# Kernel tuning notes

Hardware: AMD Instinct MI355X
Metric: run time of the kernel (lower is better)

The kernel has to match this reference:

```python
import jax, jax.numpy as jnp
import numpy as np
from jax import lax

K = 3
STRIDE = 1
PAD = 1


def _active_sites(mask):
    # mask: [B, Cm, H, W] int. A patch is 'active' if ANY element of the
    # unfolded (im2col) patch is nonzero -> max-pool of (mask != 0) over the
    # same kernel/stride/padding window.
    m = jnp.any(mask != 0, axis=1, keepdims=True).astype(jnp.float32)  # [B,1,H,W]
    pooled = lax.reduce_window(
        m, 0.0, lax.max,
        window_dimensions=(1, 1, K, K),
        window_strides=(1, 1, STRIDE, STRIDE),
        padding=((0, 0), (0, 0), (PAD, PAD), (PAD, PAD)))
    return pooled > 0  # [B,1,H_out,W_out] bool


def reference(x, mask, weight, bias):
    # Faithful math of MyConv: conv2d(x, weight) + bias at active patch sites
    # (patches whose mask window contains any nonzero), exact zeros elsewhere.
    # masked_scatter in the original preserves patch order, so this equals
    # active * (conv + bias).
    conv = lax.conv_general_dilated(
        x, weight,
        window_strides=(STRIDE, STRIDE),
        padding=((PAD, PAD), (PAD, PAD)),
        dimension_numbers=('NCHW', 'OIHW', 'NCHW'))  # [B,C_out,H_out,W_out]
    active = _active_sites(mask)
    out = (conv + bias[None, :, None, None]) * active.astype(conv.dtype)
    return out


def setup_inputs() -> dict:
    key = jax.random.key(0)
    k1, k2, k3, k4 = jax.random.split(key, 4)
    B, C_in, C_out, H, W = 8, 128, 128, 128, 128
    x = jax.random.normal(k1, (B, C_in, H, W), dtype=jnp.float32)
    mask = jax.random.randint(k2, (B, 1, H, W), 0, 2, dtype=jnp.int32)
    fan_in = C_in * K * K
    bound = 1.0 / np.sqrt(fan_in)
    weight = jax.random.uniform(k3, (C_out, C_in, K, K), minval=-bound, maxval=bound, dtype=jnp.float32)
    bias = jax.random.uniform(k4, (C_out,), minval=-bound, maxval=bound, dtype=jnp.float32)
    return {"x": x, "mask": mask, "weight": weight, "bias": bias}
```

## Files before the change

kernel.cpp:

```cpp
#include <hip/hip_runtime.h>


typedef __bf16 bf16x8 __attribute__((ext_vector_type(8)));
typedef unsigned short u16x8 __attribute__((ext_vector_type(8)));
typedef float f32x4 __attribute__((ext_vector_type(4)));

__device__ __forceinline__ unsigned short f2bf(float f) {
    unsigned int u = __float_as_uint(f);
    u += 0x7fffu + ((u >> 16) & 1u);
    return (unsigned short)(u >> 16);
}

__global__ void setup_all(const float* __restrict__ x, const float* __restrict__ wgt,
                          unsigned short* __restrict__ xp, unsigned short* __restrict__ wpp) {
    __shared__ float Lf[32 * 132];
    const int t   = threadIdx.x;
    const int bid = blockIdx.x;

    if (bid >= 4160) {
        const int e    = (bid - 4160) * 256 + t;
        const int j    = e & 31;
        const int m    = (e >> 5) & 127;
        const int r    = e >> 12;
        const int kw   = r - (r / 3) * 3;
        const int cbkh = r / 3;
        const int cb   = cbkh & 3;
        const int kh   = cbkh >> 2;
        wpp[e] = f2bf(wgt[((m * 128 + cb * 32 + j) * 3 + kh) * 3 + kw]);
        return;
    }

    const int hh2 = bid % 130;
    const int cb  = (bid / 130) & 3;
    const int b   = bid / 520;
    u16x8* slab = (u16x8*)(xp + (size_t)(((b * 4 + cb) * 130 + hh2)) * 4160);
    const u16x8 z = {0, 0, 0, 0, 0, 0, 0, 0};

    if (hh2 == 0 || hh2 == 129) {
        for (int k = t; k < 520; k += 256) slab[k] = z;
        return;
    }
    const int h = hh2 - 1;

    #pragma unroll
    for (int u = 0; u < 4; ++u) {
        const int f  = t + 256 * u;
        const int ci = f >> 5;
        const int w4 = f & 31;
        const float4 v = *(const float4*)(x + (((b * 128 + cb * 32 + ci) * 128 + h) << 7) + (w4 << 2));
        *(float4*)&Lf[ci * 132 + (w4 << 2)] = v;
    }
    __syncthreads();

    for (int k = t; k < 520; k += 256) {
        const int r = k >> 2;
        const int c = k & 3;
        u16x8 o;
        if (r == 0 || r == 129) {
            o = z;
        } else {
            const int w   = r - 1;
            const int ci0 = (c ^ ((r + (r >> 2)) & 3)) << 3;
            #pragma unroll
            for (int s = 0; s < 8; ++s) o[s] = f2bf(Lf[(ci0 + s) * 132 + w]);
        }
        slab[k] = o;
    }
}

__device__ __forceinline__ void stage_slab(const unsigned char* gx, unsigned char* ls, int t) {
    const int g    = t >> 6;
    const int lane = t & 63;
    #pragma unroll
    for (int u = 0; u < 2; ++u)
        __builtin_amdgcn_global_load_lds(
            (const __attribute__((address_space(1))) unsigned int*)(gx + u * 4096 + g * 1024 + lane * 16),
            (__attribute__((address_space(3))) unsigned int*)(ls + u * 4096 + g * 1024),
            16, 0, 0);
    if (t < 8)
        __builtin_amdgcn_global_load_lds(
            (const __attribute__((address_space(1))) unsigned int*)(gx + 8192 + t * 16),
            (__attribute__((address_space(3))) unsigned int*)(ls + 8192),
            16, 0, 0);
}

__global__ __launch_bounds__(256, 4)
void myconv6(const unsigned short* __restrict__ xp,
             const int* __restrict__ mask,
             const unsigned short* __restrict__ wp,
             const float* __restrict__ bias,
             float* __restrict__ out)
{
    __shared__ __align__(16) unsigned char Xs[2][8320];
    __shared__ float act[128];

    const int t = threadIdx.x;
    const int b = blockIdx.x >> 7;
    const int h = blockIdx.x & 127;

    const int lane = t & 63;
    const int l16  = lane & 15;
    const int q    = lane >> 4;
    const int g    = t >> 6;
    const int mh   = g & 1;
    const int nh   = g >> 1;

    const unsigned char* xpB = (const unsigned char*)xp;

    stage_slab(xpB + (size_t)((b * 4 + 0) * 130 + h + 0) * 8320, &Xs[0][0], t);

    if (t < 128) {
        int any = 0;
        #pragma unroll
        for (int kh = 0; kh < 3; ++kh) {
            int hh = h + kh - 1;
            if ((unsigned)hh < 128u) {
                const int* mrow = mask + (b * 128 + hh) * 128;
                #pragma unroll
                for (int kw = 0; kw < 3; ++kw) {
                    int ww = t + kw - 1;
                    if ((unsigned)ww < 128u) any |= mrow[ww];
                }
            }
        }
        act[t] = any ? 1.0f : 0.0f;
    }

    int bb[3];
    #pragma unroll
    for (int kw = 0; kw < 3; ++kw) {
        const int rr   = l16 + kw;
        const int slot = q ^ ((rr + (rr >> 2)) & 3);
        bb[kw] = nh * 4096 + rr * 64 + (slot << 4);
    }

    const unsigned char* agl = (const unsigned char*)wp + (mh * 64 + l16) * 64 + q * 16;

    f32x4 acc[4][4];
    const f32x4 fzero = {0.f, 0.f, 0.f, 0.f};
    #pragma unroll
    for (int i = 0; i < 4; ++i)
        #pragma unroll
        for (int j = 0; j < 4; ++j)
            acc[i][j] = fzero;

    __syncthreads();

    for (int r = 0; r < 12; ++r) {
        if (r < 11) {
            const int rn = r + 1;
            stage_slab(xpB + (size_t)((b * 4 + (rn & 3)) * 130 + h + (rn >> 2)) * 8320,
                       &Xs[(rn & 1)][0], t);
        }

        const unsigned char* ar = agl + r * 24576;
        const unsigned char* xb = &Xs[r & 1][0];
        #pragma unroll
        for (int kw = 0; kw < 3; ++kw) {
            bf16x8 af[4];
            #pragma unroll
            for (int i = 0; i < 4; ++i)
                af[i] = *(const bf16x8*)(ar + kw * 8192 + i * 1024);
            bf16x8 bfr[4];
            #pragma unroll
            for (int j = 0; j < 4; ++j)
                bfr[j] = *(const bf16x8*)(xb + bb[kw] + j * 1024);
            #pragma unroll
            for (int i = 0; i < 4; ++i)
                #pragma unroll
                for (int j = 0; j < 4; ++j)
                    acc[i][j] = __builtin_amdgcn_mfma_f32_16x16x32_bf16(af[i], bfr[j], acc[i][j], 0, 0, 0);
        }

        __syncthreads();
    }

    #pragma unroll
    for (int i = 0; i < 4; ++i) {
        const int m0 = mh * 64 + (i << 4) + (q << 2);
        const f32x4 bv = *(const f32x4*)(bias + m0);
        #pragma unroll
        for (int j = 0; j < 4; ++j) {
            const int w = nh * 64 + (j << 4) + l16;
            const float a = act[w];
            float* base = out + (((b << 7) + m0) << 14) + (h << 7) + w;
            #pragma unroll
            for (int rg = 0; rg < 4; ++rg)
                base[rg << 14] = (acc[i][j][rg] + bv[rg]) * a;
        }
    }
}

#define LDAF 40
__global__ __launch_bounds__(256, 2)
void myconv_fb(const float* __restrict__ x,
               const int* __restrict__ mask,
               const float* __restrict__ wgt,
               const float* __restrict__ bias,
               float* __restrict__ out)
{
    __shared__ unsigned short As[128 * LDAF];
    __shared__ unsigned short Bs[128 * LDAF];
    __shared__ float act[128];

    const int t   = threadIdx.x;
    const int blk = blockIdx.x;
    const int b   = blk >> 7;
    const int h   = blk & 127;

    if (t < 128) {
        int any = 0;
        #pragma unroll
        for (int kh = 0; kh < 3; ++kh) {
            int hh = h + kh - 1;
            if ((unsigned)hh < 128u) {
                const int* mrow = mask + (b * 128 + hh) * 128;
                #pragma unroll
                for (int kw = 0; kw < 3; ++kw) {
                    int ww = t + kw - 1;
                    if ((unsigned)ww < 128u) any |= mrow[ww];
                }
            }
        }
        act[t] = any ? 1.0f : 0.0f;
    }

    const int lane = t & 63;
    const int l16  = lane & 15;
    const int half = lane >> 4;
    const int wv   = t >> 6;
    const int wm   = (wv >> 1) << 6;
    const int wn   = (wv & 1) << 6;

    f32x4 acc[4][4];
    const f32x4 fzero = {0.f, 0.f, 0.f, 0.f};
    #pragma unroll
    for (int i = 0; i < 4; ++i)
        #pragma unroll
        for (int j = 0; j < 4; ++j)
            acc[i][j] = fzero;

    const int am  = t >> 3;
    const int ac4 = (t & 7) << 2;
    const int n     = t & 127;
    const int khalf = __builtin_amdgcn_readfirstlane(t >> 7);
    const int xb    = b << 21;

    for (int kt = 0; kt < 36; ++kt) {
        __syncthreads();
        #pragma unroll
        for (int jj = 0; jj < 4; ++jj) {
            const int m = am + (jj << 5);
            const float4 v = *(const float4*)(wgt + m * 1152 + kt * 32 + ac4);
            unsigned short* dst = &As[m * LDAF + ac4];
            dst[0] = f2bf(v.x); dst[1] = f2bf(v.y); dst[2] = f2bf(v.z); dst[3] = f2bf(v.w);
        }
        u16x8 bv0, bv1;
        #pragma unroll
        for (int s = 0; s < 16; ++s) {
            const int k  = kt * 32 + khalf * 16 + s;
            const int ci = (k * 7282) >> 16;
            const int r  = k - ci * 9;
            const int kh = (r >= 3) + (r >= 6);
            const int kw = r - kh * 3;
            const int hh = h + kh - 1;
            float v = 0.f;
            if ((unsigned)hh < 128u) {
                const int ww = n + kw - 1;
                if ((unsigned)ww < 128u)
                    v = x[xb + (ci << 14) + (hh << 7) + ww];
            }
            if (s < 8) bv0[s] = f2bf(v); else bv1[s - 8] = f2bf(v);
        }
        *(u16x8*)&Bs[n * LDAF + khalf * 16]     = bv0;
        *(u16x8*)&Bs[n * LDAF + khalf * 16 + 8] = bv1;

        __syncthreads();

        bf16x8 af[4], bfr[4];
        #pragma unroll
        for (int i = 0; i < 4; ++i)
            af[i] = *(const bf16x8*)&As[(wm + (i << 4) + l16) * LDAF + (half << 3)];
        #pragma unroll
        for (int j = 0; j < 4; ++j)
            bfr[j] = *(const bf16x8*)&Bs[(wn + (j << 4) + l16) * LDAF + (half << 3)];
        #pragma unroll
        for (int i = 0; i < 4; ++i)
            #pragma unroll
            for (int j = 0; j < 4; ++j)
                acc[i][j] = __builtin_amdgcn_mfma_f32_16x16x32_bf16(af[i], bfr[j], acc[i][j], 0, 0, 0);
    }

    #pragma unroll
    for (int i = 0; i < 4; ++i) {
        #pragma unroll
        for (int j = 0; j < 4; ++j) {
            const int ncol = wn + (j << 4) + l16;
            const float a  = act[ncol];
            #pragma unroll
            for (int rg = 0; rg < 4; ++rg) {
                const int m = wm + (i << 4) + (half << 2) + rg;
                out[(((b << 7) + m) << 14) + (h << 7) + ncol] =
                    (acc[i][j][rg] + bias[m]) * a;
            }
        }
    }
}

extern "C" void kernel_launch(void* const* d_in, const int* in_sizes, int n_in,
                              void* d_out, int out_size, void* d_ws, size_t ws_size,
                              hipStream_t stream) {
    const float* x    = (const float*)d_in[0];
    const int*   mask = (const int*)d_in[1];
    const float* wgt  = (const float*)d_in[2];
    const float* bias = (const float*)d_in[3];
    float* out        = (float*)d_out;

    const size_t XP_ELEMS = 4160ull * 4160;
    const size_t WP_ELEMS = 36ull * 128 * 32;
    const size_t need = (XP_ELEMS + WP_ELEMS) * 2;

    if (ws_size >= need) {
        unsigned short* xpw = (unsigned short*)d_ws;
        unsigned short* wpw = xpw + XP_ELEMS;
        setup_all<<<dim3(4736), dim3(256), 0, stream>>>(x, wgt, xpw, wpw);
        myconv6<<<dim3(1024), dim3(256), 0, stream>>>(xpw, mask, wpw, bias, out);
    } else {
        myconv_fb<<<dim3(1024), dim3(256), 0, stream>>>(x, mask, wgt, bias, out);
    }
}
```

Measured before the change: 158.8 us.

## Triple-buffer input slabs with prefetch distance two and hoisted weight loads

The conv kernel moves from double to triple buffering of the LDS input slab and prefetches two reduction steps ahead. All three kw weight fragments are loaded at the top of each step, and the loop's __syncthreads is replaced by explicit vmcnt/lgkmcnt waits plus raw barriers. The goal is to hide global-to-LDS latency behind the MFMA work. In exchange it uses more LDS and registers, lowers launch bounds occupancy from 4 to 3, and depends on a hand-counted vmcnt(18) being correct.

```diff
diff --git a/kernel.cpp b/kernel.cpp
--- a/kernel.cpp
+++ b/kernel.cpp
@@ -68,30 +68,29 @@
     }
 }
 
-__device__ __forceinline__ void stage_slab(const unsigned char* gx, unsigned char* ls, int t) {
+__device__ __forceinline__ void stage_slab3(const unsigned char* gx, unsigned char* ls, int t) {
     const int g    = t >> 6;
     const int lane = t & 63;
-    #pragma unroll
-    for (int u = 0; u < 2; ++u)
+    __builtin_amdgcn_global_load_lds(
+        (const __attribute__((address_space(1))) unsigned int*)(gx + g * 1024 + lane * 16),
+        (__attribute__((address_space(3))) unsigned int*)(ls + g * 1024), 16, 0, 0);
+    __builtin_amdgcn_global_load_lds(
+        (const __attribute__((address_space(1))) unsigned int*)(gx + 4096 + g * 1024 + lane * 16),
+        (__attribute__((address_space(3))) unsigned int*)(ls + 4096 + g * 1024), 16, 0, 0);
+    if (lane < 2)
         __builtin_amdgcn_global_load_lds(
-            (const __attribute__((address_space(1))) unsigned int*)(gx + u * 4096 + g * 1024 + lane * 16),
-            (__attribute__((address_space(3))) unsigned int*)(ls + u * 4096 + g * 1024),
-            16, 0, 0);
-    if (t < 8)
-        __builtin_amdgcn_global_load_lds(
-            (const __attribute__((address_space(1))) unsigned int*)(gx + 8192 + t * 16),
-            (__attribute__((address_space(3))) unsigned int*)(ls + 8192),
-            16, 0, 0);
-}
-
-__global__ __launch_bounds__(256, 4)
-void myconv6(const unsigned short* __restrict__ xp,
+            (const __attribute__((address_space(1))) unsigned int*)(gx + 8192 + g * 32 + lane * 16),
+            (__attribute__((address_space(3))) unsigned int*)(ls + 8192 + g * 32), 16, 0, 0);
+}
+
+__global__ __launch_bounds__(256, 3)
+void myconv7(const unsigned short* __restrict__ xp,
              const int* __restrict__ mask,
              const unsigned short* __restrict__ wp,
              const float* __restrict__ bias,
              float* __restrict__ out)
 {
-    __shared__ __align__(16) unsigned char Xs[2][8320];
+    __shared__ __align__(16) unsigned char Xs[3][8320];
     __shared__ float act[128];
 
     const int t = threadIdx.x;
@@ -106,8 +105,6 @@
     const int nh   = g >> 1;
 
     const unsigned char* xpB = (const unsigned char*)xp;
-
-    stage_slab(xpB + (size_t)((b * 4 + 0) * 130 + h + 0) * 8320, &Xs[0][0], t);
 
     if (t < 128) {
         int any = 0;
@@ -125,6 +122,10 @@
         }
         act[t] = any ? 1.0f : 0.0f;
     }
+    asm volatile("" ::: "memory");
+
+    stage_slab3(xpB + (size_t)((b * 4 + 0) * 130 + h) * 8320, &Xs[0][0], t);
+    stage_slab3(xpB + (size_t)((b * 4 + 1) * 130 + h) * 8320, &Xs[1][0], t);
 
     int bb[3];
     #pragma unroll
@@ -144,23 +145,29 @@
         for (int j = 0; j < 4; ++j)
             acc[i][j] = fzero;
 
-    __syncthreads();
-
+    int cur = 0, nx2 = 2;
     for (int r = 0; r < 12; ++r) {
-        if (r < 11) {
-            const int rn = r + 1;
-            stage_slab(xpB + (size_t)((b * 4 + (rn & 3)) * 130 + h + (rn >> 2)) * 8320,
-                       &Xs[(rn & 1)][0], t);
-        }
-
         const unsigned char* ar = agl + r * 24576;
-        const unsigned char* xb = &Xs[r & 1][0];
+        bf16x8 af[3][4];
+        #pragma unroll
+        for (int kw = 0; kw < 3; ++kw)
+            #pragma unroll
+            for (int i = 0; i < 4; ++i)
+                af[kw][i] = *(const bf16x8*)(ar + kw * 8192 + i * 1024);
+        __builtin_amdgcn_sched_barrier(0);
+
+        if (r < 10) {
+            const int rn = r + 2;
+            stage_slab3(xpB + (size_t)((b * 4 + (rn & 3)) * 130 + h + (rn >> 2)) * 8320,
+                        &Xs[nx2][0], t);
+        }
+
+        asm volatile("s_waitcnt vmcnt(18)" ::: "memory");
+        __builtin_amdgcn_s_barrier();
+
+        const unsigned char* xb = &Xs[cur][0];
         #pragma unroll
         for (int kw = 0; kw < 3; ++kw) {
-            bf16x8 af[4];
-            #pragma unroll
-            for (int i = 0; i < 4; ++i)
-                af[i] = *(const bf16x8*)(ar + kw * 8192 + i * 1024);
             bf16x8 bfr[4];
             #pragma unroll
             for (int j = 0; j < 4; ++j)
@@ -169,10 +176,15 @@
             for (int i = 0; i < 4; ++i)
                 #pragma unroll
                 for (int j = 0; j < 4; ++j)
-                    acc[i][j] = __builtin_amdgcn_mfma_f32_16x16x32_bf16(af[i], bfr[j], acc[i][j], 0, 0, 0);
-        }
-
-        __syncthreads();
+                    acc[i][j] = __builtin_amdgcn_mfma_f32_16x16x32_bf16(af[kw][i], bfr[j], acc[i][j], 0, 0, 0);
+        }
+
+        asm volatile("s_waitcnt lgkmcnt(0)" ::: "memory");
+        __builtin_amdgcn_sched_barrier(0);
+        __builtin_amdgcn_s_barrier();
+
+        cur = (cur == 2) ? 0 : cur + 1;
+        nx2 = (nx2 == 2) ? 0 : nx2 + 1;
     }
 
     #pragma unroll
@@ -324,7 +336,7 @@
         unsigned short* xpw = (unsigned short*)d_ws;
         unsigned short* wpw = xpw + XP_ELEMS;
         setup_all<<<dim3(4736), dim3(256), 0, stream>>>(x, wgt, xpw, wpw);
-        myconv6<<<dim3(1024), dim3(256), 0, stream>>>(xpw, mask, wpw, bias, out);
+        myconv7<<<dim3(1024), dim3(256), 0, stream>>>(xpw, mask, wpw, bias, out);
     } else {
         myconv_fb<<<dim3(1024), dim3(256), 0, stream>>>(x, mask, wgt, bias, out);
     }
```

New measurement: 167.2 us. 1.05x slower.

## Read input slabs directly from global memory instead of LDS double-buffering

Applied to the files above, without the earlier changes.

Removes the LDS double-buffered staging of the padded bf16 input slab (global_load_lds plus per-iteration barriers) and has each lane load its B fragments straight from global memory, relying on L1/L2 to absorb the reuse across the three kw shifts and the two M-half waves. The XOR swizzle in the setup kernel's slab layout is dropped to match the new linear addressing. Block indices are also remapped so consecutive blocks land on different batch images, which spreads work across XCDs. This trades LDS traffic and synchronisation for more global/L2 load requests and exposed load latency, with no software prefetch of the next row.

```diff
diff --git a/kernel.cpp b/kernel.cpp
--- a/kernel.cpp
+++ b/kernel.cpp
@@ -60,7 +60,7 @@
             o = z;
         } else {
             const int w   = r - 1;
-            const int ci0 = (c ^ ((r + (r >> 2)) & 3)) << 3;
+            const int ci0 = c << 3;
             #pragma unroll
             for (int s = 0; s < 8; ++s) o[s] = f2bf(Lf[(ci0 + s) * 132 + w]);
         }
@@ -68,35 +68,19 @@
     }
 }
 
-__device__ __forceinline__ void stage_slab(const unsigned char* gx, unsigned char* ls, int t) {
-    const int g    = t >> 6;
-    const int lane = t & 63;
-    #pragma unroll
-    for (int u = 0; u < 2; ++u)
-        __builtin_amdgcn_global_load_lds(
-            (const __attribute__((address_space(1))) unsigned int*)(gx + u * 4096 + g * 1024 + lane * 16),
-            (__attribute__((address_space(3))) unsigned int*)(ls + u * 4096 + g * 1024),
-            16, 0, 0);
-    if (t < 8)
-        __builtin_amdgcn_global_load_lds(
-            (const __attribute__((address_space(1))) unsigned int*)(gx + 8192 + t * 16),
-            (__attribute__((address_space(3))) unsigned int*)(ls + 8192),
-            16, 0, 0);
-}
-
 __global__ __launch_bounds__(256, 4)
-void myconv6(const unsigned short* __restrict__ xp,
+void myconv8(const unsigned short* __restrict__ xp,
              const int* __restrict__ mask,
              const unsigned short* __restrict__ wp,
              const float* __restrict__ bias,
              float* __restrict__ out)
 {
-    __shared__ __align__(16) unsigned char Xs[2][8320];
     __shared__ float act[128];
 
     const int t = threadIdx.x;
-    const int b = blockIdx.x >> 7;
-    const int h = blockIdx.x & 127;
+    const int swz = (blockIdx.x & 7) * 128 + (blockIdx.x >> 3);
+    const int b = swz >> 7;
+    const int h = swz & 127;
 
     const int lane = t & 63;
     const int l16  = lane & 15;
@@ -104,10 +88,6 @@
     const int g    = t >> 6;
     const int mh   = g & 1;
     const int nh   = g >> 1;
-
-    const unsigned char* xpB = (const unsigned char*)xp;
-
-    stage_slab(xpB + (size_t)((b * 4 + 0) * 130 + h + 0) * 8320, &Xs[0][0], t);
 
     if (t < 128) {
         int any = 0;
@@ -125,15 +105,10 @@
         }
         act[t] = any ? 1.0f : 0.0f;
     }
-
-    int bb[3];
-    #pragma unroll
-    for (int kw = 0; kw < 3; ++kw) {
-        const int rr   = l16 + kw;
-        const int slot = q ^ ((rr + (rr >> 2)) & 3);
-        bb[kw] = nh * 4096 + rr * 64 + (slot << 4);
-    }
-
+    __syncthreads();
+
+    const unsigned char* xpB = (const unsigned char*)xp;
+    const int boff = (nh * 64 + l16) * 64 + q * 16;
     const unsigned char* agl = (const unsigned char*)wp + (mh * 64 + l16) * 64 + q * 16;
 
     f32x4 acc[4][4];
@@ -144,17 +119,12 @@
         for (int j = 0; j < 4; ++j)
             acc[i][j] = fzero;
 
-    __syncthreads();
-
     for (int r = 0; r < 12; ++r) {
-        if (r < 11) {
-            const int rn = r + 1;
-            stage_slab(xpB + (size_t)((b * 4 + (rn & 3)) * 130 + h + (rn >> 2)) * 8320,
-                       &Xs[(rn & 1)][0], t);
-        }
-
+        const int cb = r & 3;
+        const int kh = r >> 2;
+        const unsigned char* xb = xpB + (size_t)((b * 4 + cb) * 130 + h + kh) * 8320 + boff;
         const unsigned char* ar = agl + r * 24576;
-        const unsigned char* xb = &Xs[r & 1][0];
+
         #pragma unroll
         for (int kw = 0; kw < 3; ++kw) {
             bf16x8 af[4];
@@ -164,15 +134,13 @@
             bf16x8 bfr[4];
             #pragma unroll
             for (int j = 0; j < 4; ++j)
-                bfr[j] = *(const bf16x8*)(xb + bb[kw] + j * 1024);
+                bfr[j] = *(const bf16x8*)(xb + kw * 64 + j * 1024);
             #pragma unroll
             for (int i = 0; i < 4; ++i)
                 #pragma unroll
                 for (int j = 0; j < 4; ++j)
                     acc[i][j] = __builtin_amdgcn_mfma_f32_16x16x32_bf16(af[i], bfr[j], acc[i][j], 0, 0, 0);
         }
-
-        __syncthreads();
     }
 
     #pragma unroll
@@ -324,7 +292,7 @@
         unsigned short* xpw = (unsigned short*)d_ws;
         unsigned short* wpw = xpw + XP_ELEMS;
         setup_all<<<dim3(4736), dim3(256), 0, stream>>>(x, wgt, xpw, wpw);
-        myconv6<<<dim3(1024), dim3(256), 0, stream>>>(xpw, mask, wpw, bias, out);
+        myconv8<<<dim3(1024), dim3(256), 0, stream>>>(xpw, mask, wpw, bias, out);
     } else {
         myconv_fb<<<dim3(1024), dim3(256), 0, stream>>>(x, mask, wgt, bias, out);
     }
```

New measurement: 186.3 us. +17.3%, slower.
